# Performance work log

Hardware: AMD Instinct MI355X
Metric: run time of the kernel (lower is better)

Reference implementation:

```python
import jax, jax.numpy as jnp
import numpy as np

B, JX, JM, D, H = 8, 2048, 2048, 512, 512
NEG_INF = -1e30


def setup_inputs() -> dict:
    key = jax.random.key(0)
    ks = jax.random.split(key, 6)
    inputs = jax.random.normal(ks[0], (B, JX, D), dtype=jnp.float32)
    memory = jax.random.normal(ks[1], (B, JM, D), dtype=jnp.float32)
    mask = jax.random.randint(ks[2], (B, JM), 0, 2, dtype=jnp.int32)
    # guarantee at least one valid memory slot per row
    mask = mask.at[:, 0].set(1)
    Wq = jax.random.normal(ks[3], (D, H), dtype=jnp.float32) * 0.05
    Wk = jax.random.normal(ks[4], (D, H), dtype=jnp.float32) * 0.05
    Wg = jax.random.normal(ks[5], (2 * D, 2 * D), dtype=jnp.float32) * 0.05
    return {"inputs": inputs, "memory": memory, "mask": mask,
            "Wq": Wq, "Wk": Wk, "Wg": Wg}


def reference(inputs, memory, mask, Wq, Wk, Wg):
    hidden = Wq.shape[-1]
    # two ReLU projections (no bias)
    q = jax.nn.relu(jnp.einsum('bxd,dh->bxh', inputs, Wq))   # [B,JX,H]
    k = jax.nn.relu(jnp.einsum('bmd,dh->bmh', memory, Wk))   # [B,JM,H]
    # scaled dot-product scores
    scores = jnp.einsum('bxh,bmh->bxm', q, k) / (hidden ** 0.5)  # [B,JX,JM]
    # softmax_mask: -inf where mask == 0 (broadcast over JX instead of tile)
    m = mask[:, None, :].astype(scores.dtype)                 # [B,1,JM]
    scores = scores * m + (1.0 - m) * NEG_INF
    logits = jax.nn.softmax(scores, axis=-1)                  # [B,JX,JM]
    # attend over RAW memory (not projected)
    att = jnp.einsum('bxm,bmd->bxd', logits, memory)          # [B,JX,D]
    # gate combiner: concat -> dense(sigmoid, no bias) -> multiply
    res = jnp.concatenate([inputs, att], axis=-1)             # [B,JX,2D]
    g = jax.nn.sigmoid(jnp.einsum('bxe,ef->bxf', res, Wg))
    return res * g
```

## Files before the change

kernel.cpp:

```cpp
#include <hip/hip_runtime.h>

typedef unsigned short u16;
typedef unsigned int   u32;

typedef short s16x8 __attribute__((ext_vector_type(8)));
typedef float f32x4 __attribute__((ext_vector_type(4)));

static __device__ __forceinline__ u16 f2bf(float f) {
  u32 u = __float_as_uint(f);
  u = (u + 0x7fffu + ((u >> 16) & 1u)) >> 16;
  return (u16)u;
}
static __device__ __forceinline__ float bf2f(u16 h) {
  return __uint_as_float(((u32)h) << 16);
}
static __device__ __forceinline__ f32x4 mfma16(s16x8 a, s16x8 b, f32x4 c) {
  return __builtin_amdgcn_mfma_f32_16x16x32_bf16(a, b, c, 0, 0, 0);
}
static __device__ __forceinline__ void gload16(const u16* g, u16* l) {
  __builtin_amdgcn_global_load_lds(
      (const __attribute__((address_space(1))) void*)g,
      (__attribute__((address_space(3))) void*)l, 16, 0, 0);
}

#define WAITVM8() asm volatile("s_waitcnt vmcnt(8)" ::: "memory")
#define WAITVM6() asm volatile("s_waitcnt vmcnt(6)" ::: "memory")
#define WAITVM0() asm volatile("s_waitcnt vmcnt(0)" ::: "memory")
#define BAR()                                  \
  do {                                         \
    asm volatile("" ::: "memory");             \
    __builtin_amdgcn_s_barrier();              \
    asm volatile("" ::: "memory");             \
  } while (0)

__global__ __launch_bounds__(256) void cvt_k(const float* __restrict__ in,
                                             u16* __restrict__ out, int n8) {
  int i = blockIdx.x * 256 + threadIdx.x;
  if (i >= n8) return;
  const float4* p = reinterpret_cast<const float4*>(in);
  float4 a = p[2 * i], b = p[2 * i + 1];
  union { u16 u[8]; uint4 v; } r;
  r.u[0] = f2bf(a.x); r.u[1] = f2bf(a.y); r.u[2] = f2bf(a.z); r.u[3] = f2bf(a.w);
  r.u[4] = f2bf(b.x); r.u[5] = f2bf(b.y); r.u[6] = f2bf(b.z); r.u[7] = f2bf(b.w);
  reinterpret_cast<uint4*>(out)[i] = r.v;
}

__global__ void cvtT_k(const float* __restrict__ in, u16* __restrict__ rm,
                       u16* __restrict__ tr) {
  __shared__ float t[32][33];
  const int z = blockIdx.z;
  const float* ip = in + (size_t)z * 2048 * 512;
  int r0 = blockIdx.y * 32, c0 = blockIdx.x * 32;
  int x = threadIdx.x, y = threadIdx.y;
  for (int i = y; i < 32; i += 8) t[i][x] = ip[(size_t)(r0 + i) * 512 + c0 + x];
  __syncthreads();
  u16* rp = rm + (size_t)z * 2048 * 512;
  u16* tp = tr + (size_t)z * 512 * 2048;
  for (int i = y; i < 32; i += 8) rp[(size_t)(r0 + i) * 512 + c0 + x] = f2bf(t[i][x]);
  for (int i = y; i < 32; i += 8) tp[(size_t)(c0 + i) * 2048 + r0 + x] = f2bf(t[x][i]);
}

__global__ void tcvt_k(const float* __restrict__ in, u16* __restrict__ out,
                       int R, int C, long long ibs, long long obs) {
  __shared__ float t[32][33];
  const float* ip = in + (size_t)blockIdx.z * ibs;
  u16* op = out + (size_t)blockIdx.z * obs;
  int r0 = blockIdx.y * 32, c0 = blockIdx.x * 32;
  int x = threadIdx.x, y = threadIdx.y;
  for (int i = y; i < 32; i += 8) t[i][x] = ip[(size_t)(r0 + i) * C + c0 + x];
  __syncthreads();
  for (int i = y; i < 32; i += 8) op[(size_t)(c0 + i) * R + r0 + x] = f2bf(t[x][i]);
}

__global__ __launch_bounds__(256) void softmax_k(u16* __restrict__ P,
                                                 const int* __restrict__ mask,
                                                 float scale) {
  __shared__ float redm[4], reds[4];
  const int row = blockIdx.x;
  const int bb = row >> 11;
  const int tid = threadIdx.x;
  u16* p = P + (size_t)row * 2048;
  const int* mk = mask + (size_t)bb * 2048;
  uint4 raw = reinterpret_cast<const uint4*>(p)[tid];
  int4 ma = reinterpret_cast<const int4*>(mk)[2 * tid];
  int4 mc = reinterpret_cast<const int4*>(mk)[2 * tid + 1];
  float v[8];
  v[0] = ma.x ? bf2f((u16)(raw.x & 0xffff)) * scale : -1e30f;
  v[1] = ma.y ? bf2f((u16)(raw.x >> 16))    * scale : -1e30f;
  v[2] = ma.z ? bf2f((u16)(raw.y & 0xffff)) * scale : -1e30f;
  v[3] = ma.w ? bf2f((u16)(raw.y >> 16))    * scale : -1e30f;
  v[4] = mc.x ? bf2f((u16)(raw.z & 0xffff)) * scale : -1e30f;
  v[5] = mc.y ? bf2f((u16)(raw.z >> 16))    * scale : -1e30f;
  v[6] = mc.z ? bf2f((u16)(raw.w & 0xffff)) * scale : -1e30f;
  v[7] = mc.w ? bf2f((u16)(raw.w >> 16))    * scale : -1e30f;
  float mx = v[0];
  #pragma unroll
  for (int i = 1; i < 8; ++i) mx = fmaxf(mx, v[i]);
  for (int off = 32; off; off >>= 1) mx = fmaxf(mx, __shfl_xor(mx, off));
  if ((tid & 63) == 0) redm[tid >> 6] = mx;
  __syncthreads();
  mx = fmaxf(fmaxf(redm[0], redm[1]), fmaxf(redm[2], redm[3]));
  float sum = 0.f;
  #pragma unroll
  for (int i = 0; i < 8; ++i) { v[i] = __expf(v[i] - mx); sum += v[i]; }
  for (int off = 32; off; off >>= 1) sum += __shfl_xor(sum, off);
  if ((tid & 63) == 0) reds[tid >> 6] = sum;
  __syncthreads();
  sum = reds[0] + reds[1] + reds[2] + reds[3];
  float inv = 1.0f / sum;
  union { u16 u[8]; uint4 q; } r;
  #pragma unroll
  for (int i = 0; i < 8; ++i) r.u[i] = f2bf(v[i] * inv);
  reinterpret_cast<uint4*>(p)[tid] = r.q;
}

template <int EPI, int NT, int NX, int NY,
          int LDA, int LDB, int LDC, int KSPLIT, int MSPLIT,
          long long ABS, long long BBS, long long CBS, int NWG>
__global__ __launch_bounds__(256, 2) void gdb(
    const u16* __restrict__ A, const u16* __restrict__ A2,
    const u16* __restrict__ Bt, const u16* __restrict__ Bt2,
    float* __restrict__ Cf, u16* __restrict__ Cb,
    const u16* __restrict__ R0, const u16* __restrict__ R1) {
  __shared__ u16 As[2][128 * 64];
  __shared__ u16 Bs[2][128 * 64];
  const int bid = blockIdx.x;
  const int wgid = (bid & 7) * (NWG / 8) + (bid >> 3);
  const int bx = wgid % NX;
  const int by = (wgid / NX) % NY;
  const int bz = wgid / (NX * NY);
  const int tid = threadIdx.x;
  const int wave = tid >> 6, lane = tid & 63;
  const int m0 = by * 128, n0 = bx * 128;
  const int wr = wave >> 1, wc = wave & 1;
  const int l15 = lane & 15, l4 = lane >> 4;
  const int srow = lane >> 3;
  const int scolsw = (((lane & 7) ^ (lane >> 3)) << 3);
  const int rsw = (l15 & 7) << 3;
  const u16* Bbase = ((m0 < MSPLIT) ? Bt : Bt2) + (size_t)bz * BBS;
  const u16* Abase0 = A + (size_t)bz * ABS;
  const u16* Abase1 = A2 + (size_t)bz * ABS;

  f32x4 acc[4][4];
  #pragma unroll
  for (int i = 0; i < 4; ++i)
    #pragma unroll
    for (int j = 0; j < 4; ++j) acc[i][j] = (f32x4){0.f, 0.f, 0.f, 0.f};

  auto stage = [&](int buf, int k0) {
    const u16* Ab;
    int kl;
    if (k0 < KSPLIT) { Ab = Abase0; kl = k0; }
    else             { Ab = Abase1; kl = k0 - KSPLIT; }
    #pragma unroll
    for (int c = 0; c < 4; ++c) {
      int chunk = wave * 4 + c;
      int row = chunk * 8 + srow;
      gload16(Ab + (size_t)(m0 + row) * LDA + kl + scolsw, &As[buf][chunk * 512]);
      gload16(Bbase + (size_t)(n0 + row) * LDB + k0 + scolsw, &Bs[buf][chunk * 512]);
    }
  };
  auto compute = [&](int cur) {
    __builtin_amdgcn_s_setprio(1);
    #pragma unroll
    for (int kk = 0; kk < 64; kk += 32) {
      s16x8 af[4], bfr[4];
      #pragma unroll
      for (int mi = 0; mi < 4; ++mi)
        af[mi] = *reinterpret_cast<const s16x8*>(
            &As[cur][(wr * 64 + mi * 16 + l15) * 64 + ((kk + l4 * 8) ^ rsw)]);
      #pragma unroll
      for (int ni = 0; ni < 4; ++ni)
        bfr[ni] = *reinterpret_cast<const s16x8*>(
            &Bs[cur][(wc * 64 + ni * 16 + l15) * 64 + ((kk + l4 * 8) ^ rsw)]);
      #pragma unroll
      for (int mi = 0; mi < 4; ++mi)
        #pragma unroll
        for (int ni = 0; ni < 4; ++ni)
          acc[mi][ni] = mfma16(af[mi], bfr[ni], acc[mi][ni]);
    }
    __builtin_amdgcn_s_setprio(0);
  };

  stage(0, 0);
  stage(1, 64);
  WAITVM8();
  BAR();
  for (int t = 0; t < NT; ++t) {
    const int cur = t & 1;
    compute(cur);
    BAR();
    if (t + 2 < NT) stage(cur, (t + 2) * 64);
    if (t + 1 < NT) {
      if (t + 2 < NT) { WAITVM8(); } else { WAITVM0(); }
      BAR();
    }
  }

  float* LF = (float*)(&As[0][0]);
  const int er = tid >> 3;
  const int ec = (tid & 7) * 16;
  #pragma unroll
  for (int mi = 0; mi < 4; ++mi) {
    __syncthreads();
    #pragma unroll
    for (int ni = 0; ni < 4; ++ni) {
      int lcol = wc * 64 + ni * 16 + l15;
      #pragma unroll
      for (int j = 0; j < 4; ++j)
        LF[(wr * 16 + l4 * 4 + j) * 132 + lcol] = acc[mi][ni][j];
    }
    __syncthreads();
    int grow = m0 + mi * 16 + (er & 15) + (er >> 4) * 64;
    int gcol = n0 + ec;
    float v[16];
    #pragma unroll
    for (int i = 0; i < 4; ++i)
      *reinterpret_cast<f32x4*>(&v[4 * i]) =
          *reinterpret_cast<const f32x4*>(&LF[er * 132 + ec + 4 * i]);
    union { u16 u[16]; uint4 q[2]; } pk;
    #pragma unroll
    for (int i = 0; i < 16; ++i)
      pk.u[i] = f2bf(EPI == 0 ? fmaxf(v[i], 0.f) : v[i]);
    u16* o = Cb + (size_t)bz * CBS + (size_t)grow * LDC + gcol;
    reinterpret_cast<uint4*>(o)[0] = pk.q[0];
    reinterpret_cast<uint4*>(o)[1] = pk.q[1];
  }
  (void)Cf; (void)R0; (void)R1;
}

template <int EPI, int NT, int NX, int NY,
          int LDA, int LDB, int LDC, int KSPLIT, int MSPLIT,
          long long ABS, long long BBS, long long CBS, int NWG>
__global__ __launch_bounds__(256, 3) void gdb64(
    const u16* __restrict__ A, const u16* __restrict__ A2,
    const u16* __restrict__ Bt, const u16* __restrict__ Bt2,
    float* __restrict__ Cf, u16* __restrict__ Cb,
    const u16* __restrict__ R0, const u16* __restrict__ R1) {
  __shared__ u16 As[2][128 * 64];
  __shared__ u16 Bs[2][64 * 64];
  const int bid = blockIdx.x;
  const int wgid = (bid & 7) * (NWG / 8) + (bid >> 3);
  const int bx = wgid % NX;
  const int by = (wgid / NX) % NY;
  const int bz = wgid / (NX * NY);
  const int tid = threadIdx.x;
  const int wave = tid >> 6, lane = tid & 63;
  const int m0 = by * 128, n0 = bx * 64;
  const int wr = wave >> 1, wc = wave & 1;
  const int l15 = lane & 15, l4 = lane >> 4;
  const int srow = lane >> 3;
  const int scolsw = (((lane & 7) ^ (lane >> 3)) << 3);
  const int rsw = (l15 & 7) << 3;
  const u16* Bbase = ((m0 < MSPLIT) ? Bt : Bt2) + (size_t)bz * BBS;
  const u16* Abase0 = A + (size_t)bz * ABS;
  const u16* Abase1 = A2 + (size_t)bz * ABS;

  f32x4 acc[4][2];
  #pragma unroll
  for (int i = 0; i < 4; ++i)
    #pragma unroll
    for (int j = 0; j < 2; ++j) acc[i][j] = (f32x4){0.f, 0.f, 0.f, 0.f};

  auto stage = [&](int buf, int k0) {
    const u16* Ab;
    int kl;
    if (k0 < KSPLIT) { Ab = Abase0; kl = k0; }
    else             { Ab = Abase1; kl = k0 - KSPLIT; }
    #pragma unroll
    for (int c = 0; c < 4; ++c) {
      int chunk = wave * 4 + c;
      int row = chunk * 8 + srow;
      gload16(Ab + (size_t)(m0 + row) * LDA + kl + scolsw, &As[buf][chunk * 512]);
    }
    #pragma unroll
    for (int c = 0; c < 2; ++c) {
      int chunk = wave * 2 + c;
      int row = chunk * 8 + srow;
      gload16(Bbase + (size_t)(n0 + row) * LDB + k0 + scolsw, &Bs[buf][chunk * 512]);
    }
  };
  auto compute = [&](int cur) {
    __builtin_amdgcn_s_setprio(1);
    #pragma unroll
    for (int kk = 0; kk < 64; kk += 32) {
      s16x8 af[4], bfr[2];
      #pragma unroll
      for (int mi = 0; mi < 4; ++mi)
        af[mi] = *reinterpret_cast<const s16x8*>(
            &As[cur][(wr * 64 + mi * 16 + l15) * 64 + ((kk + l4 * 8) ^ rsw)]);
      #pragma unroll
      for (int ni = 0; ni < 2; ++ni)
        bfr[ni] = *reinterpret_cast<const s16x8*>(
            &Bs[cur][(wc * 32 + ni * 16 + l15) * 64 + ((kk + l4 * 8) ^ rsw)]);
      #pragma unroll
      for (int mi = 0; mi < 4; ++mi)
        #pragma unroll
        for (int ni = 0; ni < 2; ++ni)
          acc[mi][ni] = mfma16(af[mi], bfr[ni], acc[mi][ni]);
    }
    __builtin_amdgcn_s_setprio(0);
  };

  stage(0, 0);
  stage(1, 64);
  WAITVM6();
  BAR();
  for (int t = 0; t < NT; ++t) {
    const int cur = t & 1;
    compute(cur);
    BAR();
    if (t + 2 < NT) stage(cur, (t + 2) * 64);
    if (t + 1 < NT) {
      if (t + 2 < NT) { WAITVM6(); } else { WAITVM0(); }
      BAR();
    }
  }

  float* LF = (float*)(&As[0][0]);
  const int er = tid >> 3;
  const int ec = (tid & 7) * 8;
  #pragma unroll
  for (int mi = 0; mi < 4; ++mi) {
    __syncthreads();
    #pragma unroll
    for (int ni = 0; ni < 2; ++ni) {
      int lc = wc * 32 + ni * 16 + l15;
      #pragma unroll
      for (int j = 0; j < 4; ++j)
        LF[(wr * 16 + l4 * 4 + j) * 68 + lc] = acc[mi][ni][j];
    }
    __syncthreads();
    int grow = m0 + (er >> 4) * 64 + mi * 16 + (er & 15);
    int gcol = n0 + ec;
    float v[8];
    #pragma unroll
    for (int i = 0; i < 2; ++i)
      *reinterpret_cast<f32x4*>(&v[4 * i]) =
          *reinterpret_cast<const f32x4*>(&LF[er * 68 + ec + 4 * i]);
    if (EPI == 3) {
      float* o = Cf + (size_t)bz * CBS + (size_t)grow * LDC + gcol;
      const u16* rb = (n0 < 512) ? (R0 + (size_t)grow * 512 + gcol)
                                 : (R1 + (size_t)grow * 512 + (gcol - 512));
      #pragma unroll
      for (int i = 0; i < 8; ++i) {
        float g = 1.0f / (1.0f + __expf(-v[i]));
        v[i] = bf2f(rb[i]) * g;
      }
      reinterpret_cast<float4*>(o)[0] = *reinterpret_cast<float4*>(&v[0]);
      reinterpret_cast<float4*>(o)[1] = *reinterpret_cast<float4*>(&v[4]);
    } else {
      union { u16 u[8]; uint4 q; } pk;
      #pragma unroll
      for (int i = 0; i < 8; ++i)
        pk.u[i] = f2bf(EPI == 0 ? fmaxf(v[i], 0.f) : v[i]);
      u16* o = Cb + (size_t)bz * CBS + (size_t)grow * LDC + gcol;
      reinterpret_cast<uint4*>(o)[0] = pk.q;
    }
  }
}

extern "C" void kernel_launch(void* const* d_in, const int* in_sizes, int n_in,
                              void* d_out, int out_size, void* d_ws, size_t ws_size,
                              hipStream_t stream) {
  const float* inputs = (const float*)d_in[0];
  const float* memory = (const float*)d_in[1];
  const int*   mask   = (const int*)d_in[2];
  const float* Wq     = (const float*)d_in[3];
  const float* Wk     = (const float*)d_in[4];
  const float* Wg     = (const float*)d_in[5];
  float* out = (float*)d_out;

  char* ws = (char*)d_ws;
  size_t off = 0;
  auto alloc = [&](size_t bytes) {
    void* p = ws + off;
    off += (bytes + 255) & ~(size_t)255;
    return p;
  };
  u16* in_b  = (u16*)alloc(16384ULL * 512 * 2);
  u16* mem_b = (u16*)alloc(16384ULL * 512 * 2);
  u16* memT  = (u16*)alloc(16384ULL * 512 * 2);
  u16* WqT   = (u16*)alloc(512ULL * 512 * 2);
  u16* WkT   = (u16*)alloc(512ULL * 512 * 2);
  u16* WgT   = (u16*)alloc(1024ULL * 1024 * 2);
  u16* q_b   = (u16*)alloc(16384ULL * 512 * 2);
  u16* k_b   = (u16*)alloc(16384ULL * 512 * 2);
  u16* sc    = (u16*)alloc(8ULL * 2048 * 2048 * 2);
  u16* att_b = (u16*)alloc(16384ULL * 512 * 2);
  (void)ws_size; (void)in_sizes; (void)n_in; (void)out_size;

  const int n8 = (16384 * 512) / 8;
  cvt_k<<<(n8 + 255) / 256, 256, 0, stream>>>(inputs, in_b, n8);
  cvtT_k<<<dim3(16, 64, 8), dim3(32, 8), 0, stream>>>(memory, mem_b, memT);
  dim3 tb(32, 8);
  tcvt_k<<<dim3(16, 16, 1), tb, 0, stream>>>(Wq, WqT, 512, 512, 0, 0);
  tcvt_k<<<dim3(16, 16, 1), tb, 0, stream>>>(Wk, WkT, 512, 512, 0, 0);
  tcvt_k<<<dim3(32, 32, 1), tb, 0, stream>>>(Wg, WgT, 1024, 1024, 0, 0);

  gdb64<0, 8, 8, 256, 512, 512, 512, (1 << 30), 16384, 0, 0, 0, 2048>
      <<<2048, 256, 0, stream>>>(in_b, in_b, WqT, WkT, nullptr, q_b,
                                 nullptr, nullptr);

  gdb<1, 8, 16, 16, 512, 512, 2048, (1 << 30), (1 << 30),
      2048LL * 512, 2048LL * 512, 2048LL * 2048, 2048>
      <<<2048, 256, 0, stream>>>(q_b, q_b, k_b, k_b, nullptr, sc,
                                 nullptr, nullptr);

  softmax_k<<<16384, 256, 0, stream>>>(sc, mask, 0.044194173824159216f);

  gdb<1, 32, 4, 16, 2048, 2048, 512, (1 << 30), (1 << 30),
      2048LL * 2048, 512LL * 2048, 2048LL * 512, 512>
      <<<512, 256, 0, stream>>>(sc, sc, memT, memT, nullptr, att_b,
                                nullptr, nullptr);

  gdb64<3, 16, 16, 128, 512, 1024, 1024, 512, (1 << 30), 0, 0, 0, 2048>
      <<<2048, 256, 0, stream>>>(in_b, att_b, WgT, WgT, out, nullptr,
                                 in_b, att_b);
}
```

Baseline: 231.2 us.

## Make GEMM workgroups persistent over several N-chunks, overlapping next A prefetch with epilogue

Replaces gdb64 with gdbc, where each workgroup walks CH consecutive 64-wide N tiles for the same 128-row M block. The next chunk's A tiles are prefetched during the current epilogue, and the epilogue staging moves into the Bs buffer so the in-flight A loads are not overwritten. The QK^T scores GEMM also switches from the 128x128 gdb to this 128x64 chunked kernel. The aim is fewer workgroups, better A reuse through cache, and hidden prologue latency. The cost is less parallelism: only 512 or 1024 blocks, each running long serial loops.

```diff
diff --git a/kernel.cpp b/kernel.cpp
--- a/kernel.cpp
+++ b/kernel.cpp
@@ -29,6 +29,12 @@
 #define BAR()                                  \
   do {                                         \
     asm volatile("" ::: "memory");             \
+    __builtin_amdgcn_s_barrier();              \
+    asm volatile("" ::: "memory");             \
+  } while (0)
+#define LBAR()                                 \
+  do {                                         \
+    asm volatile("s_waitcnt lgkmcnt(0)" ::: "memory"); \
     __builtin_amdgcn_s_barrier();              \
     asm volatile("" ::: "memory");             \
   } while (0)
@@ -114,6 +120,157 @@
   reinterpret_cast<uint4*>(p)[tid] = r.q;
 }
 
+template <int EPI, int NT, int CH, int NXC, int NY,
+          int LDA, int LDB, int LDC, int KSPLIT, int MSPLIT,
+          long long ABS, long long BBS, long long CBS, int NWG>
+__global__ __launch_bounds__(256, 3) void gdbc(
+    const u16* __restrict__ A, const u16* __restrict__ A2,
+    const u16* __restrict__ Bt, const u16* __restrict__ Bt2,
+    float* __restrict__ Cf, u16* __restrict__ Cb,
+    const u16* __restrict__ R0, const u16* __restrict__ R1) {
+  __shared__ u16 As[2][128 * 64];
+  __shared__ u16 Bs[2][64 * 64];
+  const int bid = blockIdx.x;
+  const int wgid = (bid & 7) * (NWG / 8) + (bid >> 3);
+  const int bxc = wgid % NXC;
+  const int by = (wgid / NXC) % NY;
+  const int bz = wgid / (NXC * NY);
+  const int tid = threadIdx.x;
+  const int wave = tid >> 6, lane = tid & 63;
+  const int m0 = by * 128;
+  const int wr = wave >> 1, wc = wave & 1;
+  const int l15 = lane & 15, l4 = lane >> 4;
+  const int srow = lane >> 3;
+  const int scolsw = (((lane & 7) ^ (lane >> 3)) << 3);
+  const int rsw = (l15 & 7) << 3;
+  const u16* Bbase = ((m0 < MSPLIT) ? Bt : Bt2) + (size_t)bz * BBS;
+  const u16* Abase0 = A + (size_t)bz * ABS;
+  const u16* Abase1 = A2 + (size_t)bz * ABS;
+
+  f32x4 acc[4][2];
+
+  auto stageA = [&](int buf, int k0) {
+    const u16* Ab;
+    int kl;
+    if (k0 < KSPLIT) { Ab = Abase0; kl = k0; }
+    else             { Ab = Abase1; kl = k0 - KSPLIT; }
+    #pragma unroll
+    for (int c = 0; c < 4; ++c) {
+      int chunk = wave * 4 + c;
+      int row = chunk * 8 + srow;
+      gload16(Ab + (size_t)(m0 + row) * LDA + kl + scolsw, &As[buf][chunk * 512]);
+    }
+  };
+  auto stageB = [&](int buf, int k0, int n0) {
+    #pragma unroll
+    for (int c = 0; c < 2; ++c) {
+      int chunk = wave * 2 + c;
+      int row = chunk * 8 + srow;
+      gload16(Bbase + (size_t)(n0 + row) * LDB + k0 + scolsw, &Bs[buf][chunk * 512]);
+    }
+  };
+  auto compute = [&](int cur) {
+    __builtin_amdgcn_s_setprio(1);
+    #pragma unroll
+    for (int kk = 0; kk < 64; kk += 32) {
+      s16x8 af[4], bfr[2];
+      #pragma unroll
+      for (int mi = 0; mi < 4; ++mi)
+        af[mi] = *reinterpret_cast<const s16x8*>(
+            &As[cur][(wr * 64 + mi * 16 + l15) * 64 + ((kk + l4 * 8) ^ rsw)]);
+      #pragma unroll
+      for (int ni = 0; ni < 2; ++ni)
+        bfr[ni] = *reinterpret_cast<const s16x8*>(
+            &Bs[cur][(wc * 32 + ni * 16 + l15) * 64 + ((kk + l4 * 8) ^ rsw)]);
+      #pragma unroll
+      for (int mi = 0; mi < 4; ++mi)
+        #pragma unroll
+        for (int ni = 0; ni < 2; ++ni)
+          acc[mi][ni] = mfma16(af[mi], bfr[ni], acc[mi][ni]);
+    }
+    __builtin_amdgcn_s_setprio(0);
+  };
+
+  {
+    const int n00 = bxc * CH * 64;
+    stageA(0, 0); stageB(0, 0, n00);
+    stageA(1, 64); stageB(1, 64, n00);
+    WAITVM6();
+    BAR();
+  }
+
+  #pragma unroll 1
+  for (int s = 0; s < CH; ++s) {
+    const int n0 = (bxc * CH + s) * 64;
+    #pragma unroll
+    for (int i = 0; i < 4; ++i)
+      #pragma unroll
+      for (int j = 0; j < 2; ++j) acc[i][j] = (f32x4){0.f, 0.f, 0.f, 0.f};
+
+    for (int t = 0; t < NT; ++t) {
+      const int cur = t & 1;
+      compute(cur);
+      BAR();
+      if (t + 2 < NT) { stageA(cur, (t + 2) * 64); stageB(cur, (t + 2) * 64, n0); }
+      if (t + 1 < NT) {
+        if (t + 2 < NT) { WAITVM6(); } else { WAITVM0(); }
+        BAR();
+      }
+    }
+    if (s + 1 < CH) { stageA(0, 0); stageA(1, 64); }
+
+    {
+      float* LF = (float*)(&Bs[0][0]);
+      const int er = tid >> 3;
+      const int ec = (tid & 7) * 8;
+      #pragma unroll
+      for (int mi = 0; mi < 4; ++mi) {
+        LBAR();
+        #pragma unroll
+        for (int ni = 0; ni < 2; ++ni) {
+          int lc = wc * 32 + ni * 16 + l15;
+          #pragma unroll
+          for (int j = 0; j < 4; ++j)
+            LF[(wr * 16 + l4 * 4 + j) * 68 + lc] = acc[mi][ni][j];
+        }
+        LBAR();
+        int grow = m0 + (er >> 4) * 64 + mi * 16 + (er & 15);
+        int gcol = n0 + ec;
+        float v[8];
+        #pragma unroll
+        for (int i = 0; i < 2; ++i)
+          *reinterpret_cast<f32x4*>(&v[4 * i]) =
+              *reinterpret_cast<const f32x4*>(&LF[er * 68 + ec + 4 * i]);
+        if (EPI == 3) {
+          float* o = Cf + (size_t)bz * CBS + (size_t)grow * LDC + gcol;
+          const u16* rb = (gcol < 512) ? (R0 + (size_t)grow * 512 + gcol)
+                                       : (R1 + (size_t)grow * 512 + (gcol - 512));
+          #pragma unroll
+          for (int i = 0; i < 8; ++i) {
+            float g = 1.0f / (1.0f + __expf(-v[i]));
+            v[i] = bf2f(rb[i]) * g;
+          }
+          reinterpret_cast<float4*>(o)[0] = *reinterpret_cast<float4*>(&v[0]);
+          reinterpret_cast<float4*>(o)[1] = *reinterpret_cast<float4*>(&v[4]);
+        } else {
+          union { u16 u[8]; uint4 q; } pk;
+          #pragma unroll
+          for (int i = 0; i < 8; ++i)
+            pk.u[i] = f2bf(EPI == 0 ? fmaxf(v[i], 0.f) : v[i]);
+          u16* o = Cb + (size_t)bz * CBS + (size_t)grow * LDC + gcol;
+          reinterpret_cast<uint4*>(o)[0] = pk.q;
+        }
+      }
+    }
+    if (s + 1 < CH) {
+      const int nn = (bxc * CH + s + 1) * 64;
+      stageB(0, 0, nn); stageB(1, 64, nn);
+      WAITVM0();
+      BAR();
+    }
+  }
+}
+
 template <int EPI, int NT, int NX, int NY,
           int LDA, int LDB, int LDC, int KSPLIT, int MSPLIT,
           long long ABS, long long BBS, long long CBS, int NWG>
@@ -229,137 +386,6 @@
   (void)Cf; (void)R0; (void)R1;
 }
 
-template <int EPI, int NT, int NX, int NY,
-          int LDA, int LDB, int LDC, int KSPLIT, int MSPLIT,
-          long long ABS, long long BBS, long long CBS, int NWG>
-__global__ __launch_bounds__(256, 3) void gdb64(
-    const u16* __restrict__ A, const u16* __restrict__ A2,
-    const u16* __restrict__ Bt, const u16* __restrict__ Bt2,
-    float* __restrict__ Cf, u16* __restrict__ Cb,
-    const u16* __restrict__ R0, const u16* __restrict__ R1) {
-  __shared__ u16 As[2][128 * 64];
-  __shared__ u16 Bs[2][64 * 64];
-  const int bid = blockIdx.x;
-  const int wgid = (bid & 7) * (NWG / 8) + (bid >> 3);
-  const int bx = wgid % NX;
-  const int by = (wgid / NX) % NY;
-  const int bz = wgid / (NX * NY);
-  const int tid = threadIdx.x;
-  const int wave = tid >> 6, lane = tid & 63;
-  const int m0 = by * 128, n0 = bx * 64;
-  const int wr = wave >> 1, wc = wave & 1;
-  const int l15 = lane & 15, l4 = lane >> 4;
-  const int srow = lane >> 3;
-  const int scolsw = (((lane & 7) ^ (lane >> 3)) << 3);
-  const int rsw = (l15 & 7) << 3;
-  const u16* Bbase = ((m0 < MSPLIT) ? Bt : Bt2) + (size_t)bz * BBS;
-  const u16* Abase0 = A + (size_t)bz * ABS;
-  const u16* Abase1 = A2 + (size_t)bz * ABS;
-
-  f32x4 acc[4][2];
-  #pragma unroll
-  for (int i = 0; i < 4; ++i)
-    #pragma unroll
-    for (int j = 0; j < 2; ++j) acc[i][j] = (f32x4){0.f, 0.f, 0.f, 0.f};
-
-  auto stage = [&](int buf, int k0) {
-    const u16* Ab;
-    int kl;
-    if (k0 < KSPLIT) { Ab = Abase0; kl = k0; }
-    else             { Ab = Abase1; kl = k0 - KSPLIT; }
-    #pragma unroll
-    for (int c = 0; c < 4; ++c) {
-      int chunk = wave * 4 + c;
-      int row = chunk * 8 + srow;
-      gload16(Ab + (size_t)(m0 + row) * LDA + kl + scolsw, &As[buf][chunk * 512]);
-    }
-    #pragma unroll
-    for (int c = 0; c < 2; ++c) {
-      int chunk = wave * 2 + c;
-      int row = chunk * 8 + srow;
-      gload16(Bbase + (size_t)(n0 + row) * LDB + k0 + scolsw, &Bs[buf][chunk * 512]);
-    }
-  };
-  auto compute = [&](int cur) {
-    __builtin_amdgcn_s_setprio(1);
-    #pragma unroll
-    for (int kk = 0; kk < 64; kk += 32) {
-      s16x8 af[4], bfr[2];
-      #pragma unroll
-      for (int mi = 0; mi < 4; ++mi)
-        af[mi] = *reinterpret_cast<const s16x8*>(
-            &As[cur][(wr * 64 + mi * 16 + l15) * 64 + ((kk + l4 * 8) ^ rsw)]);
-      #pragma unroll
-      for (int ni = 0; ni < 2; ++ni)
-        bfr[ni] = *reinterpret_cast<const s16x8*>(
-            &Bs[cur][(wc * 32 + ni * 16 + l15) * 64 + ((kk + l4 * 8) ^ rsw)]);
-      #pragma unroll
-      for (int mi = 0; mi < 4; ++mi)
-        #pragma unroll
-        for (int ni = 0; ni < 2; ++ni)
-          acc[mi][ni] = mfma16(af[mi], bfr[ni], acc[mi][ni]);
-    }
-    __builtin_amdgcn_s_setprio(0);
-  };
-
-  stage(0, 0);
-  stage(1, 64);
-  WAITVM6();
-  BAR();
-  for (int t = 0; t < NT; ++t) {
-    const int cur = t & 1;
-    compute(cur);
-    BAR();
-    if (t + 2 < NT) stage(cur, (t + 2) * 64);
-    if (t + 1 < NT) {
-      if (t + 2 < NT) { WAITVM6(); } else { WAITVM0(); }
-      BAR();
-    }
-  }
-
-  float* LF = (float*)(&As[0][0]);
-  const int er = tid >> 3;
-  const int ec = (tid & 7) * 8;
-  #pragma unroll
-  for (int mi = 0; mi < 4; ++mi) {
-    __syncthreads();
-    #pragma unroll
-    for (int ni = 0; ni < 2; ++ni) {
-      int lc = wc * 32 + ni * 16 + l15;
-      #pragma unroll
-      for (int j = 0; j < 4; ++j)
-        LF[(wr * 16 + l4 * 4 + j) * 68 + lc] = acc[mi][ni][j];
-    }
-    __syncthreads();
-    int grow = m0 + (er >> 4) * 64 + mi * 16 + (er & 15);
-    int gcol = n0 + ec;
-    float v[8];
-    #pragma unroll
-    for (int i = 0; i < 2; ++i)
-      *reinterpret_cast<f32x4*>(&v[4 * i]) =
-          *reinterpret_cast<const f32x4*>(&LF[er * 68 + ec + 4 * i]);
-    if (EPI == 3) {
-      float* o = Cf + (size_t)bz * CBS + (size_t)grow * LDC + gcol;
-      const u16* rb = (n0 < 512) ? (R0 + (size_t)grow * 512 + gcol)
-                                 : (R1 + (size_t)grow * 512 + (gcol - 512));
-      #pragma unroll
-      for (int i = 0; i < 8; ++i) {
-        float g = 1.0f / (1.0f + __expf(-v[i]));
-        v[i] = bf2f(rb[i]) * g;
-      }
-      reinterpret_cast<float4*>(o)[0] = *reinterpret_cast<float4*>(&v[0]);
-      reinterpret_cast<float4*>(o)[1] = *reinterpret_cast<float4*>(&v[4]);
-    } else {
-      union { u16 u[8]; uint4 q; } pk;
-      #pragma unroll
-      for (int i = 0; i < 8; ++i)
-        pk.u[i] = f2bf(EPI == 0 ? fmaxf(v[i], 0.f) : v[i]);
-      u16* o = Cb + (size_t)bz * CBS + (size_t)grow * LDC + gcol;
-      reinterpret_cast<uint4*>(o)[0] = pk.q;
-    }
-  }
-}
-
 extern "C" void kernel_launch(void* const* d_in, const int* in_sizes, int n_in,
                               void* d_out, int out_size, void* d_ws, size_t ws_size,
                               hipStream_t stream) {
@@ -398,13 +424,13 @@
   tcvt_k<<<dim3(16, 16, 1), tb, 0, stream>>>(Wk, WkT, 512, 512, 0, 0);
   tcvt_k<<<dim3(32, 32, 1), tb, 0, stream>>>(Wg, WgT, 1024, 1024, 0, 0);
 
-  gdb64<0, 8, 8, 256, 512, 512, 512, (1 << 30), 16384, 0, 0, 0, 2048>
-      <<<2048, 256, 0, stream>>>(in_b, in_b, WqT, WkT, nullptr, q_b,
-                                 nullptr, nullptr);
-
-  gdb<1, 8, 16, 16, 512, 512, 2048, (1 << 30), (1 << 30),
-      2048LL * 512, 2048LL * 512, 2048LL * 2048, 2048>
-      <<<2048, 256, 0, stream>>>(q_b, q_b, k_b, k_b, nullptr, sc,
+  gdbc<0, 8, 4, 2, 256, 512, 512, 512, (1 << 30), 16384, 0, 0, 0, 512>
+      <<<512, 256, 0, stream>>>(in_b, in_b, WqT, WkT, nullptr, q_b,
+                                nullptr, nullptr);
+
+  gdbc<1, 8, 4, 8, 16, 512, 512, 2048, (1 << 30), (1 << 30),
+       2048LL * 512, 2048LL * 512, 2048LL * 2048, 1024>
+      <<<1024, 256, 0, stream>>>(q_b, q_b, k_b, k_b, nullptr, sc,
                                  nullptr, nullptr);
 
   softmax_k<<<16384, 256, 0, stream>>>(sc, mask, 0.044194173824159216f);
@@ -414,7 +440,7 @@
       <<<512, 256, 0, stream>>>(sc, sc, memT, memT, nullptr, att_b,
                                 nullptr, nullptr);
 
-  gdb64<3, 16, 16, 128, 512, 1024, 1024, 512, (1 << 30), 0, 0, 0, 2048>
-      <<<2048, 256, 0, stream>>>(in_b, att_b, WgT, WgT, out, nullptr,
-                                 in_b, att_b);
-}
+  gdbc<3, 16, 4, 4, 128, 512, 1024, 1024, 512, (1 << 30), 0, 0, 0, 512>
+      <<<512, 256, 0, stream>>>(in_b, att_b, WgT, WgT, out, nullptr,
+                                in_b, att_b);
+}
```

Measured after the change: 309.2 us. 1.34x slower.
